# Kernel optimization log

Measured on AMD Instinct MI355X. Metric: run time of the kernel, lower is better.

## Reference

```python
import jax, jax.numpy as jnp
import numpy as np

B, C, H, W = 8, 64, 64, 64
OUT = 256
N_PAIRS = C * (C + 1) // 2          # 2080 upper-triangular (incl diag) products
N_IN = C + N_PAIRS                  # 2144 conv input channels


def setup_inputs() -> dict:
    key = jax.random.key(0)
    k1, k2 = jax.random.split(key)
    x = jax.random.normal(k1, (B, C, H, W), dtype=jnp.float32)
    fc_w = jax.random.normal(k2, (OUT, N_IN), dtype=jnp.float32) * 0.02
    return {"x": x, "fc_w": fc_w}


def reference(x, fc_w):
    # Upper-triangular indices (row-major, incl diagonal) == get_square_indices(C)
    ii, jj = np.triu_indices(x.shape[1])
    # Per-pixel outer product restricted to the needed triangular terms.
    quad = x[:, ii] * x[:, jj]                  # [B, C(C+1)/2, H, W]
    y = jnp.concatenate([x, quad], axis=1)      # [B, C(C+3)/2, H, W]
    # 1x1 conv, bias=False -> pointwise channel GEMM
    return jnp.einsum('bchw,oc->bohw', y, fc_w)
```

## Files before the change

kernel.cpp:

```cpp
#include <hip/hip_runtime.h>
#include <hip/hip_bf16.h>

using u16 = unsigned short;
using u32 = unsigned int;

typedef __attribute__((ext_vector_type(8)))  short s16x8;
typedef __attribute__((ext_vector_type(4)))  float f32x4;
typedef __attribute__((ext_vector_type(16))) float f32x16;
typedef __attribute__((ext_vector_type(4)))  u32   u32x4;

#define NQ 74
#define WG_U16   (NQ * 2 * 4096)
#define RUNPK_OFF (WG_U16 * 2)

__device__ __forceinline__ u16 f2bf_rne(float f) {
    u32 u = __builtin_bit_cast(u32, f);
    u32 r = u + 0x7fffu + ((u >> 16) & 1u);
    return (u16)(r >> 16);
}
__device__ __forceinline__ float bf2f(u16 u) {
    u32 v = ((u32)u) << 16;
    return __builtin_bit_cast(float, v);
}

__device__ __forceinline__ void run_decode(int r, int& i, int& j0) {
    if (r < 8) { i = 64; j0 = r << 3; return; }
    int rr = r - 8;
    int ii = 0;
    while (true) { int cnt = 8 - (ii >> 3); if (rr < cnt) break; rr -= cnt; ++ii; }
    i = ii;
    j0 = ((ii >> 3) << 3) + (rr << 3);
}

__global__ __launch_bounds__(1024)
void pack_w(const float* __restrict__ fcw, u16* __restrict__ wg,
            u32* __restrict__ runpk) {
    if (blockIdx.x == 0 && threadIdx.x < NQ * 2) {
        int q = threadIdx.x >> 1, ks = threadIdx.x & 1;
        int i0, j00, i1, j01;
        run_decode(q * 4 + ks * 2 + 0, i0, j00);
        run_decode(q * 4 + ks * 2 + 1, i1, j01);
        runpk[threadIdx.x] =
            ((u32)i0 << 24) | ((u32)j00 << 16) | ((u32)i1 << 8) | (u32)j01;
    }
    const u32 g  = blockIdx.x * 1024 + threadIdx.x;
    const int e  = g & 7;
    const int l  = (g >> 3) & 63;
    const int ks = (g >> 9) & 1;
    const int ni = (g >> 10) & 3;
    const int nh = (g >> 12) & 1;
    const int q  = g >> 13;
    const int kh = l >> 5;
    int i, j0; run_decode(q * 4 + ks * 2 + kh, i, j0);
    const int n = nh * 128 + ni * 32 + (l & 31);
    const int j = j0 + e;
    float w;
    if (i == 64)    w = fcw[n * 2144 + j];
    else if (j < i) w = 0.f;
    else            w = fcw[n * 2144 + 64 + i * 64 - ((i * (i - 1)) >> 1) + (j - i)];
    wg[g] = f2bf_rne(w);
}

__device__ __forceinline__ s16x8 packmul(float fi, s16x8 vj) {
    u32 pk[4];
    #pragma unroll
    for (int d = 0; d < 4; ++d) {
        float p0 = fi * bf2f((u16)vj[2 * d]);
        float p1 = fi * bf2f((u16)vj[2 * d + 1]);
        pk[d] = __builtin_amdgcn_perm(__builtin_bit_cast(u32, p1),
                                      __builtin_bit_cast(u32, p0), 0x07060302u);
    }
    u32x4 pv = { pk[0], pk[1], pk[2], pk[3] };
    return __builtin_bit_cast(s16x8, pv);
}

__global__ __launch_bounds__(512, 2)
void quad_gemm(const float* __restrict__ x, const s16x8* __restrict__ wg16,
               const u32* __restrict__ runpk, float* __restrict__ out) {
    __shared__ __align__(16) u16   x_lds[256 * 64];
    __shared__ __align__(16) u16   x_t[64 * 256];
    __shared__ __align__(16) s16x8 wbuf[3][512];
    __shared__ u32 runl[NQ * 2];

    const int t   = threadIdx.x;
    const int l   = t & 63;
    const int wv  = t >> 6;
    const int rr  = wv >> 1;
    const int cc  = wv & 1;
    const int kh  = l >> 5;
    const int lm  = l & 31;
    const int sw8 = (l & 7) << 3;

    const int mtile = blockIdx.x >> 1;
    const int nb    = blockIdx.x & 1;
    const int pix0  = mtile * 256;
    const int b     = pix0 >> 12;
    const int hw0   = pix0 & 4095;

    if (t < NQ * 2) runl[t] = runpk[t];

    {
        const int mg = (t & 63) << 2;
        const int cg = (t >> 6) << 3;
        const float* xp = x + ((size_t)b << 18) + hw0 + mg;
        f32x4 vv[8];
        #pragma unroll
        for (int e = 0; e < 8; ++e)
            vv[e] = *(const f32x4*)(xp + ((size_t)(cg + e) << 12));
        u16 tb[8][4];
        #pragma unroll
        for (int e = 0; e < 8; ++e)
            #pragma unroll
            for (int r = 0; r < 4; ++r) tb[e][r] = f2bf_rne(vv[e][r]);
        #pragma unroll
        for (int r = 0; r < 4; ++r) {
            int m = mg + r;
            s16x8 pv = { (short)tb[0][r], (short)tb[1][r], (short)tb[2][r],
                         (short)tb[3][r], (short)tb[4][r], (short)tb[5][r],
                         (short)tb[6][r], (short)tb[7][r] };
            *(s16x8*)(x_lds + (m << 6) + (cg ^ ((m & 7) << 3))) = pv;
        }
        #pragma unroll
        for (int e = 0; e < 8; ++e) {
            typedef __attribute__((ext_vector_type(4))) short s16x4;
            s16x4 pv = { (short)tb[e][0], (short)tb[e][1],
                         (short)tb[e][2], (short)tb[e][3] };
            *(s16x4*)(x_t + ((cg + e) << 8) + mg) = pv;
        }
    }

    char* wb0 = (char*)&wbuf[0][0];
    char* wb1 = (char*)&wbuf[1][0];
    char* wb2 = (char*)&wbuf[2][0];
    const s16x8* wsrc = wg16 + nb * 512 + t;

    #define STAGEQ(Q, DST) __builtin_amdgcn_global_load_lds(                 \
        (const __attribute__((address_space(1))) void*)(wsrc + (size_t)(Q) * 1024), \
        (__attribute__((address_space(3))) void*)((DST) + wv * 1024), 16, 0, 0)

    STAGEQ(0, wb0);
    STAGEQ(1, wb1);

    const int xrow0 = (rr * 64 + lm) << 6;
    const int xrow1 = (rr * 64 + 32 + lm) << 6;
    const int mt0   = rr * 64 + lm;

    f32x16 acc00, acc01, acc10, acc11;
    #pragma unroll
    for (int r = 0; r < 16; ++r) {
        acc00[r] = 0.f; acc01[r] = 0.f; acc10[r] = 0.f; acc11[r] = 0.f;
    }

    #define GENQ(Q, Y00_, Y01_, Y10_, Y11_) do {                             \
        u32 rp0_ = runl[(Q) * 2], rp1_ = runl[(Q) * 2 + 1];                  \
        u32 ij0_ = kh ? (rp0_ & 0xffffu) : (rp0_ >> 16);                     \
        u32 ij1_ = kh ? (rp1_ & 0xffffu) : (rp1_ >> 16);                     \
        int ia_ = (int)(ij0_ >> 8), ja_ = (int)(ij0_ & 255u) ^ sw8;          \
        int ib_ = (int)(ij1_ >> 8), jb_ = (int)(ij1_ & 255u) ^ sw8;         \
        float fa0_ = (ia_ >= 64) ? 1.0f : bf2f(x_t[((ia_ & 63) << 8) + mt0]);      \
        float fa1_ = (ia_ >= 64) ? 1.0f : bf2f(x_t[((ia_ & 63) << 8) + mt0 + 32]); \
        float fb0_ = (ib_ >= 64) ? 1.0f : bf2f(x_t[((ib_ & 63) << 8) + mt0]);      \
        float fb1_ = (ib_ >= 64) ? 1.0f : bf2f(x_t[((ib_ & 63) << 8) + mt0 + 32]); \
        Y00_ = packmul(fa0_, *(const s16x8*)(x_lds + xrow0 + ja_));          \
        Y10_ = packmul(fa1_, *(const s16x8*)(x_lds + xrow1 + ja_));          \
        Y01_ = packmul(fb0_, *(const s16x8*)(x_lds + xrow0 + jb_));          \
        Y11_ = packmul(fb1_, *(const s16x8*)(x_lds + xrow1 + jb_));          \
    } while (0)

    asm volatile("s_waitcnt lgkmcnt(0)" ::: "memory");
    __builtin_amdgcn_s_barrier();
    asm volatile("" ::: "memory");

    s16x8 Y00, Y01, Y10, Y11;
    GENQ(0, Y00, Y01, Y10, Y11);

    for (int q = 0; q < NQ; ++q) {
        if (q == NQ - 1) { asm volatile("s_waitcnt vmcnt(0)" ::: "memory"); }
        else             { asm volatile("s_waitcnt vmcnt(1)" ::: "memory"); }
        __builtin_amdgcn_s_barrier();
        asm volatile("" ::: "memory");

        const s16x8* wbp = (const s16x8*)wb0;
        s16x8 W00 = wbp[(cc * 4 + 0) * 64 + l];
        s16x8 W01 = wbp[(cc * 4 + 1) * 64 + l];
        s16x8 W10 = wbp[(cc * 4 + 2) * 64 + l];
        s16x8 W11 = wbp[(cc * 4 + 3) * 64 + l];

        if (q < NQ - 2) STAGEQ(q + 2, wb2);

        acc00 = __builtin_amdgcn_mfma_f32_32x32x16_bf16(W00, Y00, acc00, 0, 0, 0);
        acc00 = __builtin_amdgcn_mfma_f32_32x32x16_bf16(W01, Y01, acc00, 0, 0, 0);
        acc01 = __builtin_amdgcn_mfma_f32_32x32x16_bf16(W10, Y00, acc01, 0, 0, 0);
        acc01 = __builtin_amdgcn_mfma_f32_32x32x16_bf16(W11, Y01, acc01, 0, 0, 0);
        acc10 = __builtin_amdgcn_mfma_f32_32x32x16_bf16(W00, Y10, acc10, 0, 0, 0);
        acc10 = __builtin_amdgcn_mfma_f32_32x32x16_bf16(W01, Y11, acc10, 0, 0, 0);
        acc11 = __builtin_amdgcn_mfma_f32_32x32x16_bf16(W10, Y10, acc11, 0, 0, 0);
        acc11 = __builtin_amdgcn_mfma_f32_32x32x16_bf16(W11, Y11, acc11, 0, 0, 0);

        if (q < NQ - 1) GENQ(q + 1, Y00, Y01, Y10, Y11);

        char* tmpp = wb0; wb0 = wb1; wb1 = wb2; wb2 = tmpp;
    }

    float* ob = out + ((size_t)b << 20) + (size_t)hw0;
    const int ob0 = nb * 128 + cc * 64 + kh * 4;
    #pragma unroll
    for (int r = 0; r < 16; ++r) {
        const int o = ob0 + (r & 3) + 8 * (r >> 2);
        ob[(size_t)o * 4096 + mt0]             = acc00[r];
        ob[(size_t)(o + 32) * 4096 + mt0]      = acc01[r];
        ob[(size_t)o * 4096 + mt0 + 32]        = acc10[r];
        ob[(size_t)(o + 32) * 4096 + mt0 + 32] = acc11[r];
    }
}

extern "C" void kernel_launch(void* const* d_in, const int* in_sizes, int n_in,
                              void* d_out, int out_size, void* d_ws, size_t ws_size,
                              hipStream_t stream) {
    const float* x   = (const float*)d_in[0];
    const float* fcw = (const float*)d_in[1];
    float* out = (float*)d_out;
    u16* wg    = (u16*)d_ws;
    u32* runpk = (u32*)((char*)d_ws + RUNPK_OFF);

    hipLaunchKernelGGL(pack_w, dim3(WG_U16 / 1024), dim3(1024), 0, stream,
                       fcw, wg, runpk);
    hipLaunchKernelGGL(quad_gemm, dim3(256), dim3(512), 0, stream,
                       x, (const s16x8*)wg, runpk, out);
}
```

Baseline: 132.3 us.

## Halve pixel tile to 128, double grid, drop transposed x copy

The main GEMM now gives each block 128 pixels instead of 256 and launches 512 blocks with a launch-bounds hint of 4 blocks per CU. Each wave now owns one 32-pixel row with two accumulators instead of four, and the transposed x_t buffer is gone: the scalar factor is read from the swizzled x_lds row. The loop is unrolled by two with ping-pong Y registers, and the next products are generated before the MFMAs. pack_w now decodes runs once per block into shared memory instead of once per thread. The aim is more parallelism and occupancy with less LDS, at the cost of less weight reuse per block, so twice as much weight traffic goes through LDS.

```diff
diff --git a/kernel.cpp b/kernel.cpp
--- a/kernel.cpp
+++ b/kernel.cpp
@@ -5,7 +5,7 @@
 using u32 = unsigned int;
 
 typedef __attribute__((ext_vector_type(8)))  short s16x8;
-typedef __attribute__((ext_vector_type(4)))  float f32x4;
+typedef __attribute__((ext_vector_type(2)))  float f32x2;
 typedef __attribute__((ext_vector_type(16))) float f32x16;
 typedef __attribute__((ext_vector_type(4)))  u32   u32x4;
 
@@ -35,23 +35,30 @@
 __global__ __launch_bounds__(1024)
 void pack_w(const float* __restrict__ fcw, u16* __restrict__ wg,
             u32* __restrict__ runpk) {
-    if (blockIdx.x == 0 && threadIdx.x < NQ * 2) {
-        int q = threadIdx.x >> 1, ks = threadIdx.x & 1;
-        int i0, j00, i1, j01;
-        run_decode(q * 4 + ks * 2 + 0, i0, j00);
-        run_decode(q * 4 + ks * 2 + 1, i1, j01);
-        runpk[threadIdx.x] =
-            ((u32)i0 << 24) | ((u32)j00 << 16) | ((u32)i1 << 8) | (u32)j01;
-    }
-    const u32 g  = blockIdx.x * 1024 + threadIdx.x;
+    __shared__ u16 runs4[4];
+    const int q = blockIdx.x >> 3;
+    const int t = threadIdx.x;
+    if (t < 4) {
+        int i, j0; run_decode(q * 4 + t, i, j0);
+        runs4[t] = (u16)((i << 8) | j0);
+        if ((blockIdx.x & 7) == 0 && t < 2) {
+            int ia, ja, ib, jb;
+            run_decode(q * 4 + t * 2 + 0, ia, ja);
+            run_decode(q * 4 + t * 2 + 1, ib, jb);
+            runpk[q * 2 + t] =
+                ((u32)ia << 24) | ((u32)ja << 16) | ((u32)ib << 8) | (u32)jb;
+        }
+    }
+    __syncthreads();
+    const u32 g  = blockIdx.x * 1024 + t;
     const int e  = g & 7;
     const int l  = (g >> 3) & 63;
     const int ks = (g >> 9) & 1;
     const int ni = (g >> 10) & 3;
     const int nh = (g >> 12) & 1;
-    const int q  = g >> 13;
     const int kh = l >> 5;
-    int i, j0; run_decode(q * 4 + ks * 2 + kh, i, j0);
+    const u16 ij = runs4[ks * 2 + kh];
+    const int i = ij >> 8, j0 = ij & 255;
     const int n = nh * 128 + ni * 32 + (l & 31);
     const int j = j0 + e;
     float w;
@@ -74,143 +81,114 @@
     return __builtin_bit_cast(s16x8, pv);
 }
 
-__global__ __launch_bounds__(512, 2)
-void quad_gemm(const float* __restrict__ x, const s16x8* __restrict__ wg16,
+__global__ __launch_bounds__(512, 4)
+void quad_gemm(const float* __restrict__ x, const u16* __restrict__ wg,
                const u32* __restrict__ runpk, float* __restrict__ out) {
-    __shared__ __align__(16) u16   x_lds[256 * 64];
-    __shared__ __align__(16) u16   x_t[64 * 256];
-    __shared__ __align__(16) s16x8 wbuf[3][512];
+    __shared__ __align__(16) u16 x_lds[128 * 64];
+    __shared__ __align__(16) u16 wbuf[3][4096];
     __shared__ u32 runl[NQ * 2];
 
     const int t   = threadIdx.x;
     const int l   = t & 63;
     const int wv  = t >> 6;
-    const int rr  = wv >> 1;
-    const int cc  = wv & 1;
+    const int mrow = wv >> 1;
+    const int nc   = wv & 1;
     const int kh  = l >> 5;
     const int lm  = l & 31;
-    const int sw8 = (l & 7) << 3;
+    const int sw8 = (lm & 7) << 3;
 
     const int mtile = blockIdx.x >> 1;
     const int nb    = blockIdx.x & 1;
-    const int pix0  = mtile * 256;
+    const int pix0  = mtile * 128;
     const int b     = pix0 >> 12;
     const int hw0   = pix0 & 4095;
 
     if (t < NQ * 2) runl[t] = runpk[t];
 
     {
-        const int mg = (t & 63) << 2;
+        const int mg = (t & 63) << 1;
         const int cg = (t >> 6) << 3;
         const float* xp = x + ((size_t)b << 18) + hw0 + mg;
-        f32x4 vv[8];
+        f32x2 vv[8];
         #pragma unroll
         for (int e = 0; e < 8; ++e)
-            vv[e] = *(const f32x4*)(xp + ((size_t)(cg + e) << 12));
-        u16 tb[8][4];
+            vv[e] = *(const f32x2*)(xp + ((size_t)(cg + e) << 12));
         #pragma unroll
-        for (int e = 0; e < 8; ++e)
-            #pragma unroll
-            for (int r = 0; r < 4; ++r) tb[e][r] = f2bf_rne(vv[e][r]);
-        #pragma unroll
-        for (int r = 0; r < 4; ++r) {
+        for (int r = 0; r < 2; ++r) {
             int m = mg + r;
-            s16x8 pv = { (short)tb[0][r], (short)tb[1][r], (short)tb[2][r],
-                         (short)tb[3][r], (short)tb[4][r], (short)tb[5][r],
-                         (short)tb[6][r], (short)tb[7][r] };
+            s16x8 pv = { (short)f2bf_rne(vv[0][r]), (short)f2bf_rne(vv[1][r]),
+                         (short)f2bf_rne(vv[2][r]), (short)f2bf_rne(vv[3][r]),
+                         (short)f2bf_rne(vv[4][r]), (short)f2bf_rne(vv[5][r]),
+                         (short)f2bf_rne(vv[6][r]), (short)f2bf_rne(vv[7][r]) };
             *(s16x8*)(x_lds + (m << 6) + (cg ^ ((m & 7) << 3))) = pv;
         }
-        #pragma unroll
-        for (int e = 0; e < 8; ++e) {
-            typedef __attribute__((ext_vector_type(4))) short s16x4;
-            s16x4 pv = { (short)tb[e][0], (short)tb[e][1],
-                         (short)tb[e][2], (short)tb[e][3] };
-            *(s16x4*)(x_t + ((cg + e) << 8) + mg) = pv;
-        }
-    }
-
+    }
+
+    const u16* wsrc = wg + (size_t)nb * 4096 + t * 8;
     char* wb0 = (char*)&wbuf[0][0];
     char* wb1 = (char*)&wbuf[1][0];
     char* wb2 = (char*)&wbuf[2][0];
-    const s16x8* wsrc = wg16 + nb * 512 + t;
-
-    #define STAGEQ(Q, DST) __builtin_amdgcn_global_load_lds(                 \
-        (const __attribute__((address_space(1))) void*)(wsrc + (size_t)(Q) * 1024), \
-        (__attribute__((address_space(3))) void*)((DST) + wv * 1024), 16, 0, 0)
-
+    #define STAGEQ(Q, DST) __builtin_amdgcn_global_load_lds(                  \
+        (const __attribute__((address_space(1))) void*)(wsrc + (size_t)(Q) * 8192), \
+        (__attribute__((address_space(3))) void*)((DST) + t * 16), 16, 0, 0)
     STAGEQ(0, wb0);
     STAGEQ(1, wb1);
 
-    const int xrow0 = (rr * 64 + lm) << 6;
-    const int xrow1 = (rr * 64 + 32 + lm) << 6;
-    const int mt0   = rr * 64 + lm;
-
-    f32x16 acc00, acc01, acc10, acc11;
+    const int xrow = (mrow * 32 + lm) << 6;
+
+    f32x16 acc0, acc1;
     #pragma unroll
-    for (int r = 0; r < 16; ++r) {
-        acc00[r] = 0.f; acc01[r] = 0.f; acc10[r] = 0.f; acc11[r] = 0.f;
-    }
-
-    #define GENQ(Q, Y00_, Y01_, Y10_, Y11_) do {                             \
+    for (int r = 0; r < 16; ++r) { acc0[r] = 0.f; acc1[r] = 0.f; }
+
+    #define GENQ(Q, Y0_, Y1_) do {                                           \
         u32 rp0_ = runl[(Q) * 2], rp1_ = runl[(Q) * 2 + 1];                  \
         u32 ij0_ = kh ? (rp0_ & 0xffffu) : (rp0_ >> 16);                     \
         u32 ij1_ = kh ? (rp1_ & 0xffffu) : (rp1_ >> 16);                     \
         int ia_ = (int)(ij0_ >> 8), ja_ = (int)(ij0_ & 255u) ^ sw8;          \
-        int ib_ = (int)(ij1_ >> 8), jb_ = (int)(ij1_ & 255u) ^ sw8;         \
-        float fa0_ = (ia_ >= 64) ? 1.0f : bf2f(x_t[((ia_ & 63) << 8) + mt0]);      \
-        float fa1_ = (ia_ >= 64) ? 1.0f : bf2f(x_t[((ia_ & 63) << 8) + mt0 + 32]); \
-        float fb0_ = (ib_ >= 64) ? 1.0f : bf2f(x_t[((ib_ & 63) << 8) + mt0]);      \
-        float fb1_ = (ib_ >= 64) ? 1.0f : bf2f(x_t[((ib_ & 63) << 8) + mt0 + 32]); \
-        Y00_ = packmul(fa0_, *(const s16x8*)(x_lds + xrow0 + ja_));          \
-        Y10_ = packmul(fa1_, *(const s16x8*)(x_lds + xrow1 + ja_));          \
-        Y01_ = packmul(fb0_, *(const s16x8*)(x_lds + xrow0 + jb_));          \
-        Y11_ = packmul(fb1_, *(const s16x8*)(x_lds + xrow1 + jb_));          \
+        int ib_ = (int)(ij1_ >> 8), jb_ = (int)(ij1_ & 255u) ^ sw8;          \
+        float fa_ = (ia_ >= 64) ? 1.0f : bf2f(x_lds[xrow + ((ia_ & 63) ^ sw8)]); \
+        float fb_ = (ib_ >= 64) ? 1.0f : bf2f(x_lds[xrow + ((ib_ & 63) ^ sw8)]); \
+        Y0_ = packmul(fa_, *(const s16x8*)(x_lds + xrow + ja_));             \
+        Y1_ = packmul(fb_, *(const s16x8*)(x_lds + xrow + jb_));             \
     } while (0)
 
-    asm volatile("s_waitcnt lgkmcnt(0)" ::: "memory");
-    __builtin_amdgcn_s_barrier();
-    asm volatile("" ::: "memory");
-
-    s16x8 Y00, Y01, Y10, Y11;
-    GENQ(0, Y00, Y01, Y10, Y11);
-
-    for (int q = 0; q < NQ; ++q) {
-        if (q == NQ - 1) { asm volatile("s_waitcnt vmcnt(0)" ::: "memory"); }
-        else             { asm volatile("s_waitcnt vmcnt(1)" ::: "memory"); }
-        __builtin_amdgcn_s_barrier();
-        asm volatile("" ::: "memory");
-
-        const s16x8* wbp = (const s16x8*)wb0;
-        s16x8 W00 = wbp[(cc * 4 + 0) * 64 + l];
-        s16x8 W01 = wbp[(cc * 4 + 1) * 64 + l];
-        s16x8 W10 = wbp[(cc * 4 + 2) * 64 + l];
-        s16x8 W11 = wbp[(cc * 4 + 3) * 64 + l];
-
-        if (q < NQ - 2) STAGEQ(q + 2, wb2);
-
-        acc00 = __builtin_amdgcn_mfma_f32_32x32x16_bf16(W00, Y00, acc00, 0, 0, 0);
-        acc00 = __builtin_amdgcn_mfma_f32_32x32x16_bf16(W01, Y01, acc00, 0, 0, 0);
-        acc01 = __builtin_amdgcn_mfma_f32_32x32x16_bf16(W10, Y00, acc01, 0, 0, 0);
-        acc01 = __builtin_amdgcn_mfma_f32_32x32x16_bf16(W11, Y01, acc01, 0, 0, 0);
-        acc10 = __builtin_amdgcn_mfma_f32_32x32x16_bf16(W00, Y10, acc10, 0, 0, 0);
-        acc10 = __builtin_amdgcn_mfma_f32_32x32x16_bf16(W01, Y11, acc10, 0, 0, 0);
-        acc11 = __builtin_amdgcn_mfma_f32_32x32x16_bf16(W10, Y10, acc11, 0, 0, 0);
-        acc11 = __builtin_amdgcn_mfma_f32_32x32x16_bf16(W11, Y11, acc11, 0, 0, 0);
-
-        if (q < NQ - 1) GENQ(q + 1, Y00, Y01, Y10, Y11);
-
-        char* tmpp = wb0; wb0 = wb1; wb1 = wb2; wb2 = tmpp;
-    }
+    #define STEP(Q, YC0, YC1, YN0, YN1, LAST) do {                           \
+        if (LAST) { asm volatile("s_waitcnt vmcnt(0)" ::: "memory"); }       \
+        else      { asm volatile("s_waitcnt vmcnt(1)" ::: "memory"); }       \
+        __builtin_amdgcn_s_barrier();                                        \
+        asm volatile("" ::: "memory");                                       \
+        if ((Q) + 2 < NQ) STAGEQ((Q) + 2, wb2);                              \
+        const s16x8* wbp_ = (const s16x8*)wb0;                               \
+        s16x8 W00_ = wbp_[(nc * 4 + 0) * 64 + l];                            \
+        s16x8 W01_ = wbp_[(nc * 4 + 1) * 64 + l];                            \
+        s16x8 W10_ = wbp_[(nc * 4 + 2) * 64 + l];                            \
+        s16x8 W11_ = wbp_[(nc * 4 + 3) * 64 + l];                            \
+        if (!(LAST)) GENQ((Q) + 1, YN0, YN1);                                \
+        acc0 = __builtin_amdgcn_mfma_f32_32x32x16_bf16(W00_, YC0, acc0, 0, 0, 0); \
+        acc0 = __builtin_amdgcn_mfma_f32_32x32x16_bf16(W01_, YC1, acc0, 0, 0, 0); \
+        acc1 = __builtin_amdgcn_mfma_f32_32x32x16_bf16(W10_, YC0, acc1, 0, 0, 0); \
+        acc1 = __builtin_amdgcn_mfma_f32_32x32x16_bf16(W11_, YC1, acc1, 0, 0, 0); \
+        char* tp_ = wb0; wb0 = wb1; wb1 = wb2; wb2 = tp_;                    \
+    } while (0)
+
+    __syncthreads();
+
+    s16x8 Ya0, Ya1, Yb0, Yb1;
+    GENQ(0, Ya0, Ya1);
+    for (int q = 0; q < NQ - 2; q += 2) {
+        STEP(q,     Ya0, Ya1, Yb0, Yb1, false);
+        STEP(q + 1, Yb0, Yb1, Ya0, Ya1, false);
+    }
+    STEP(NQ - 2, Ya0, Ya1, Yb0, Yb1, false);
+    STEP(NQ - 1, Yb0, Yb1, Ya0, Ya1, true);
 
     float* ob = out + ((size_t)b << 20) + (size_t)hw0;
-    const int ob0 = nb * 128 + cc * 64 + kh * 4;
+    const int px = mrow * 32 + lm;
     #pragma unroll
     for (int r = 0; r < 16; ++r) {
-        const int o = ob0 + (r & 3) + 8 * (r >> 2);
-        ob[(size_t)o * 4096 + mt0]             = acc00[r];
-        ob[(size_t)(o + 32) * 4096 + mt0]      = acc01[r];
-        ob[(size_t)o * 4096 + mt0 + 32]        = acc10[r];
-        ob[(size_t)(o + 32) * 4096 + mt0 + 32] = acc11[r];
+        const int o = nb * 128 + nc * 64 + kh * 4 + (r & 3) + 8 * (r >> 2);
+        ob[(size_t)o * 4096 + px]        = acc0[r];
+        ob[(size_t)(o + 32) * 4096 + px] = acc1[r];
     }
 }
 
@@ -225,6 +203,6 @@
 
     hipLaunchKernelGGL(pack_w, dim3(WG_U16 / 1024), dim3(1024), 0, stream,
                        fcw, wg, runpk);
-    hipLaunchKernelGGL(quad_gemm, dim3(256), dim3(512), 0, stream,
-                       x, (const s16x8*)wg, runpk, out);
-}
+    hipLaunchKernelGGL(quad_gemm, dim3(512), dim3(512), 0, stream,
+                       x, wg, runpk, out);
+}
```

Result: faster. 129.0 us (-2.5%).
